# Kernel tuning notes

Hardware: AMD Instinct MI355X
Metric: run time of the kernel (lower is better)

## Reference

```python
import jax, jax.numpy as jnp
import numpy as np


def setup_inputs() -> dict:
    key = jax.random.key(0)
    k1, k2, k3 = jax.random.split(key, 3)
    B, T, F = 16, 2048, 64
    he = jax.random.normal(k1, (B, T, F), dtype=jnp.float32)
    scale = 1.0 / np.sqrt(F).astype(np.float32)
    W1 = jax.random.normal(k2, (F, F), dtype=jnp.float32) * scale
    W2 = jax.random.normal(k3, (F, F), dtype=jnp.float32) * scale
    return {"he": he, "W1": W1, "W2": W2, "attention_len": 48}


def reference(he, W1, W2, attention_len):
    # he: [B, T, F] encoder states. For each output step i the original module:
    #   1) unrolls L_i = min(attention_len, max(i,1)) decoder steps starting
    #      from he[:, i, :]:  H_k = sigmoid(H_{k-1} @ W1), Y_k = sigmoid(H_k @ W2)
    #   2) attends Y_1..Y_{L_i} against the encoder window he[:, i-L_i:i, :]
    #      with per-step dot-product scores, softmax over the window, and a
    #      weighted sum of the encoder window.
    # (i=0 degenerates to a single-element softmax -> context = he[:, 0, :].)
    B, T, F = he.shape
    A = attention_len

    def step(H, _):
        H = jax.nn.sigmoid(H @ W1)          # [B, T, F]
        Y = jax.nn.sigmoid(H @ W2)          # [B, T, F]
        return H, Y

    # Decoder outputs for every start position, all A steps: Ys[b, i, t, f]
    _, Ys = jax.lax.scan(step, he, None, length=A)   # [A, B, T, F]
    Ys = jnp.moveaxis(Ys, 0, 2)                      # [B, T, A, F]

    i = jnp.arange(T)[:, None]                       # [T, 1]
    t = jnp.arange(A)[None, :]                       # [1, A]
    L = jnp.minimum(A, jnp.maximum(i, 1))            # window length per step
    j = jnp.clip(i - L + t, 0, T - 1)                # encoder index per (i, t)
    valid = t < L                                    # [T, A]

    gathered = he[:, j, :]                           # [B, T, A, F] windowed encoder
    scores = jnp.einsum('btaf,btaf->bta', Ys, gathered)
    scores = jnp.where(valid[None, :, :], scores, jnp.float32(-1e9))
    w = jax.nn.softmax(scores, axis=-1)              # [B, T, A]
    ctx = jnp.einsum('bta,btaf->btf', w, gathered)   # [B, T, F]
    return ctx
```

## Files before the change

kernel.cpp:

```cpp
#include <hip/hip_runtime.h>

#define B_   16
#define T_   2048
#define F_   64
#define A_   48
#define TOK  64
#define WSTR 68
#define HWS  72
#define SSTR 49
#define NWIN 111

typedef __attribute__((ext_vector_type(4))) _Float16 half4;
typedef __attribute__((ext_vector_type(2))) _Float16 half2;
typedef __attribute__((ext_vector_type(4))) float    f32x4;

#define LOG2E 1.4426950408889634f

__device__ __forceinline__ float sigp(float c) {
    return __builtin_amdgcn_rcpf(1.0f + __builtin_amdgcn_exp2f(c));
}
__device__ __forceinline__ half2 pk2(float a, float b) {
    return __builtin_bit_cast(half2, __builtin_amdgcn_cvt_pkrtz(a, b));
}
__device__ __forceinline__ half4 sigpack(f32x4 c) {
    half2 lo = pk2(sigp(c[0]), sigp(c[1]));
    half2 hi = pk2(sigp(c[2]), sigp(c[3]));
    half4 h; h[0] = lo[0]; h[1] = lo[1]; h[2] = hi[0]; h[3] = hi[1];
    return h;
}

__device__ __forceinline__ void gemm4(const half4 (&aW)[4][4], const half4 (&hb)[4], f32x4 (&c)[4]) {
#pragma unroll
    for (int mo = 0; mo < 4; ++mo) {
        f32x4 z = {0.f, 0.f, 0.f, 0.f};
#pragma unroll
        for (int kt = 0; kt < 4; ++kt)
            z = __builtin_amdgcn_mfma_f32_16x16x16f16(aW[mo][kt], hb[kt], z, 0, 0, 0);
        c[mo] = z;
    }
}

struct Smem {
    float    sWin[NWIN * WSTR];
    _Float16 sWinH[NWIN * HWS];
    float    sSc[TOK * SSTR];
};

template<bool FIRST>
__device__ __forceinline__ void run_block(Smem& sm, int b, int t0,
                                          const float* __restrict__ he,
                                          const float* __restrict__ W1,
                                          const float* __restrict__ W2,
                                          float* __restrict__ out)
{
    const int tid = threadIdx.x;
    const float* __restrict__ heB = he + (size_t)b * T_ * F_;

    for (int i = tid; i < NWIN * 16; i += 256) {
        int row = i >> 4, c4 = (i & 15) * 4;
        int g = t0 - 48 + row;
        if (!FIRST || g >= 0) {
            float4 v = *(const float4*)(heB + (size_t)g * F_ + c4);
            *(float4*)(&sm.sWin[row * WSTR + c4]) = v;
            half2 lo = pk2(v.x, v.y), hi = pk2(v.z, v.w);
            half4 h; h[0] = lo[0]; h[1] = lo[1]; h[2] = hi[0]; h[3] = hi[1];
            *(half4*)(&sm.sWinH[row * HWS + c4]) = h;
        }
    }

    const int lane = tid & 63;
    const int wv   = tid >> 6;
    const int quad = lane >> 4;
    const int ml   = lane & 15;
    const int tw0  = wv * 16;
    const int tg   = t0 + tw0 + ml;
    const int L    = min(A_, max(tg, 1));

    half4 aW1[4][4], aW2[4][4];
    for (int mo = 0; mo < 4; ++mo)
        for (int kt = 0; kt < 4; ++kt) {
            half4 f1, f2;
#pragma unroll
            for (int j = 0; j < 4; ++j) {
                int k = kt * 16 + quad * 4 + j;
                f1[j] = (_Float16)(-LOG2E * W1[k * F_ + mo * 16 + ml]);
                f2[j] = (_Float16)(-LOG2E * W2[k * F_ + mo * 16 + ml]);
            }
            aW1[mo][kt] = f1; aW2[mo][kt] = f2;
        }

    half4 hb[4];
#pragma unroll
    for (int kt = 0; kt < 4; ++kt) {
        float4 v = *(const float4*)(heB + (size_t)tg * F_ + kt * 16 + quad * 4);
        half4 h;
        h[0] = (_Float16)v.x; h[1] = (_Float16)v.y;
        h[2] = (_Float16)v.z; h[3] = (_Float16)v.w;
        hb[kt] = h;
    }

    f32x4 c1[4];
    gemm4(aW1, hb, c1);

    __syncthreads();

    const bool amDiag = (quad == (ml >> 2));
    const bool s0 = (ml & 3) == 0, s1 = (ml & 3) == 1, s2 = (ml & 3) == 2;
    float* scp = &sm.sSc[(tw0 + ml) * SSTR];

    const _Float16* __restrict__ wbase = &sm.sWinH[(tw0 + ml) * HWS + quad * 4];

    auto wp_for = [&](int a2) -> const _Float16* {
        if (FIRST) {
            int j = tg - L + a2; if (j < 0) j = 0;
            return &sm.sWinH[(j + 48) * HWS + quad * 4];
        }
        return wbase + a2 * HWS;
    };

    half4 g0, g1, g2, g3;
    {
        const _Float16* wp = wp_for(0);
        g0 = *(const half4*)(wp);
        g1 = *(const half4*)(wp + 16);
        g2 = *(const half4*)(wp + 32);
        g3 = *(const half4*)(wp + 48);
    }

#pragma unroll 4
    for (int a = 0; a < A_; ++a) {
#pragma unroll
        for (int mo = 0; mo < 4; ++mo) hb[mo] = sigpack(c1[mo]);

        f32x4 c2[4];
        gemm4(aW2, hb, c2);
        gemm4(aW1, hb, c1);

        half4 n0, n1, n2, n3;
        {
            int an = (a + 1 < A_) ? a + 1 : A_ - 1;
            const _Float16* wp = wp_for(an);
            n0 = *(const half4*)(wp);
            n1 = *(const half4*)(wp + 16);
            n2 = *(const half4*)(wp + 32);
            n3 = *(const half4*)(wp + 48);
        }

        half4 yh[4];
#pragma unroll
        for (int mo = 0; mo < 4; ++mo) yh[mo] = sigpack(c2[mo]);

        f32x4 za = {0.f, 0.f, 0.f, 0.f}, zb = {0.f, 0.f, 0.f, 0.f};
        za = __builtin_amdgcn_mfma_f32_16x16x16f16(yh[0], g0, za, 0, 0, 0);
        zb = __builtin_amdgcn_mfma_f32_16x16x16f16(yh[1], g1, zb, 0, 0, 0);
        za = __builtin_amdgcn_mfma_f32_16x16x16f16(yh[2], g2, za, 0, 0, 0);
        zb = __builtin_amdgcn_mfma_f32_16x16x16f16(yh[3], g3, zb, 0, 0, 0);
        f32x4 zs = za + zb;
        float val = s0 ? zs[0] : (s1 ? zs[1] : (s2 ? zs[2] : zs[3]));
        if (FIRST) val = (a < L) ? val : -1e9f;
        if (amDiag) scp[a] = val;

        g0 = n0; g1 = n1; g2 = n2; g3 = n3;
    }
    __syncthreads();

    {
        int r = tid >> 2, s = tid & 3;
        float sc[12];
#pragma unroll
        for (int i = 0; i < 12; ++i) sc[i] = sm.sSc[r * SSTR + i * 4 + s];
        float m = sc[0];
#pragma unroll
        for (int i = 1; i < 12; ++i) m = fmaxf(m, sc[i]);
        m = fmaxf(m, __shfl_xor(m, 1));
        m = fmaxf(m, __shfl_xor(m, 2));
        float e[12]; float sum = 0.f;
#pragma unroll
        for (int i = 0; i < 12; ++i) { e[i] = __expf(sc[i] - m); sum += e[i]; }
        sum += __shfl_xor(sum, 1);
        sum += __shfl_xor(sum, 2);
        float inv = __builtin_amdgcn_rcpf(sum);
#pragma unroll
        for (int i = 0; i < 12; ++i) sm.sSc[r * SSTR + i * 4 + s] = e[i] * inv;
    }
    __syncthreads();

    {
        int r = tid >> 2, fc = (tid & 3) * 16;
        int tgr = t0 + r;
        int Lr = min(A_, max(tgr, 1));
        float acc[16];
#pragma unroll
        for (int q = 0; q < 16; ++q) acc[q] = 0.f;
        for (int a = 0; a < A_; ++a) {
            float wgt = sm.sSc[r * SSTR + a];
            int j = tgr - Lr + a;
            if (FIRST) { if (j < 0) j = 0; }
            const float* wp = &sm.sWin[(j - t0 + 48) * WSTR + fc];
#pragma unroll
            for (int q = 0; q < 4; ++q) {
                float4 g = *(const float4*)(wp + q * 4);
                acc[q*4+0] += wgt * g.x; acc[q*4+1] += wgt * g.y;
                acc[q*4+2] += wgt * g.z; acc[q*4+3] += wgt * g.w;
            }
        }
        float* op = out + ((size_t)b * T_ + tgr) * F_ + fc;
#pragma unroll
        for (int q = 0; q < 4; ++q)
            *(float4*)(op + q * 4) = make_float4(acc[q*4], acc[q*4+1], acc[q*4+2], acc[q*4+3]);
    }
}

__global__ __launch_bounds__(256)
void ContextBlock_kernel(const float* __restrict__ he, const float* __restrict__ W1,
                         const float* __restrict__ W2, float* __restrict__ out)
{
    __shared__ Smem sm;
    const int blk = blockIdx.x;
    if (blk < B_ * 31) {
        int b  = blk / 31;
        int t0 = ((blk % 31) + 1) * TOK;
        run_block<false>(sm, b, t0, he, W1, W2, out);
    } else {
        int b = blk - B_ * 31;
        run_block<true>(sm, b, 0, he, W1, W2, out);
    }
}

extern "C" void kernel_launch(void* const* d_in, const int* in_sizes, int n_in,
                              void* d_out, int out_size, void* d_ws, size_t ws_size,
                              hipStream_t stream) {
    const float* he = (const float*)d_in[0];
    const float* W1 = (const float*)d_in[1];
    const float* W2 = (const float*)d_in[2];
    float* out = (float*)d_out;
    hipLaunchKernelGGL(ContextBlock_kernel, dim3(512), dim3(256), 0, stream, he, W1, W2, out);
}
```

Measured before the change: 124.9 us.

## Process two token groups per wave to interleave independent MFMA recurrence chains

Each wave now handles 32 tokens as two independent 16-token groups, interleaving their sigmoid/MFMA recurrence chains to hide dependency latency within a wave. The block size is halved to 128 threads, and the window load, softmax and weighted-sum phases are remapped to cover 64 tokens with fewer threads. This trades thread-level parallelism and occupancy for instruction-level parallelism and higher register use per thread.

```diff
diff --git a/kernel.cpp b/kernel.cpp
--- a/kernel.cpp
+++ b/kernel.cpp
@@ -56,7 +56,7 @@
     const int tid = threadIdx.x;
     const float* __restrict__ heB = he + (size_t)b * T_ * F_;
 
-    for (int i = tid; i < NWIN * 16; i += 256) {
+    for (int i = tid; i < NWIN * 16; i += 128) {
         int row = i >> 4, c4 = (i & 15) * 4;
         int g = t0 - 48 + row;
         if (!FIRST || g >= 0) {
@@ -72,9 +72,11 @@
     const int wv   = tid >> 6;
     const int quad = lane >> 4;
     const int ml   = lane & 15;
-    const int tw0  = wv * 16;
-    const int tg   = t0 + tw0 + ml;
-    const int L    = min(A_, max(tg, 1));
+    const int tw0  = wv * 32;
+    const int tgA  = t0 + tw0 + ml;
+    const int tgB  = tgA + 16;
+    const int LA   = min(A_, max(tgA, 1));
+    const int LB   = min(A_, max(tgB, 1));
 
     half4 aW1[4][4], aW2[4][4];
     for (int mo = 0; mo < 4; ++mo)
@@ -89,116 +91,157 @@
             aW1[mo][kt] = f1; aW2[mo][kt] = f2;
         }
 
-    half4 hb[4];
+    half4 hbA[4], hbB[4];
 #pragma unroll
     for (int kt = 0; kt < 4; ++kt) {
-        float4 v = *(const float4*)(heB + (size_t)tg * F_ + kt * 16 + quad * 4);
+        float4 v = *(const float4*)(heB + (size_t)tgA * F_ + kt * 16 + quad * 4);
         half4 h;
         h[0] = (_Float16)v.x; h[1] = (_Float16)v.y;
         h[2] = (_Float16)v.z; h[3] = (_Float16)v.w;
-        hb[kt] = h;
-    }
-
-    f32x4 c1[4];
-    gemm4(aW1, hb, c1);
+        hbA[kt] = h;
+        float4 w = *(const float4*)(heB + (size_t)tgB * F_ + kt * 16 + quad * 4);
+        half4 g;
+        g[0] = (_Float16)w.x; g[1] = (_Float16)w.y;
+        g[2] = (_Float16)w.z; g[3] = (_Float16)w.w;
+        hbB[kt] = g;
+    }
+
+    f32x4 c1A[4], c1B[4];
+    gemm4(aW1, hbA, c1A);
+    gemm4(aW1, hbB, c1B);
 
     __syncthreads();
 
     const bool amDiag = (quad == (ml >> 2));
     const bool s0 = (ml & 3) == 0, s1 = (ml & 3) == 1, s2 = (ml & 3) == 2;
-    float* scp = &sm.sSc[(tw0 + ml) * SSTR];
-
-    const _Float16* __restrict__ wbase = &sm.sWinH[(tw0 + ml) * HWS + quad * 4];
-
-    auto wp_for = [&](int a2) -> const _Float16* {
+    float* scpA = &sm.sSc[(tw0 + ml) * SSTR];
+    float* scpB = &sm.sSc[(tw0 + 16 + ml) * SSTR];
+
+    const _Float16* __restrict__ wbaseA = &sm.sWinH[(tw0 + ml) * HWS + quad * 4];
+    const _Float16* __restrict__ wbaseB = &sm.sWinH[(tw0 + 16 + ml) * HWS + quad * 4];
+
+    auto wpA_for = [&](int a2) -> const _Float16* {
         if (FIRST) {
-            int j = tg - L + a2; if (j < 0) j = 0;
+            int j = tgA - LA + a2; if (j < 0) j = 0;
             return &sm.sWinH[(j + 48) * HWS + quad * 4];
         }
-        return wbase + a2 * HWS;
+        return wbaseA + a2 * HWS;
     };
-
-    half4 g0, g1, g2, g3;
+    auto wpB_for = [&](int a2) -> const _Float16* {
+        if (FIRST) {
+            int j = tgB - LB + a2; if (j < 0) j = 0;
+            return &sm.sWinH[(j + 48) * HWS + quad * 4];
+        }
+        return wbaseB + a2 * HWS;
+    };
+
+    half4 gA0, gA1, gA2, gA3, gB0, gB1, gB2, gB3;
     {
-        const _Float16* wp = wp_for(0);
-        g0 = *(const half4*)(wp);
-        g1 = *(const half4*)(wp + 16);
-        g2 = *(const half4*)(wp + 32);
-        g3 = *(const half4*)(wp + 48);
-    }
-
-#pragma unroll 4
+        const _Float16* wp = wpA_for(0);
+        gA0 = *(const half4*)(wp);
+        gA1 = *(const half4*)(wp + 16);
+        gA2 = *(const half4*)(wp + 32);
+        gA3 = *(const half4*)(wp + 48);
+        wp = wpB_for(0);
+        gB0 = *(const half4*)(wp);
+        gB1 = *(const half4*)(wp + 16);
+        gB2 = *(const half4*)(wp + 32);
+        gB3 = *(const half4*)(wp + 48);
+    }
+
+#pragma unroll 2
     for (int a = 0; a < A_; ++a) {
 #pragma unroll
-        for (int mo = 0; mo < 4; ++mo) hb[mo] = sigpack(c1[mo]);
-
-        f32x4 c2[4];
-        gemm4(aW2, hb, c2);
-        gemm4(aW1, hb, c1);
-
-        half4 n0, n1, n2, n3;
+        for (int mo = 0; mo < 4; ++mo) hbA[mo] = sigpack(c1A[mo]);
+#pragma unroll
+        for (int mo = 0; mo < 4; ++mo) hbB[mo] = sigpack(c1B[mo]);
+
+        f32x4 c2A[4], c2B[4];
+        gemm4(aW2, hbA, c2A);
+        gemm4(aW2, hbB, c2B);
+        gemm4(aW1, hbA, c1A);
+        gemm4(aW1, hbB, c1B);
+
+        int an = (a + 1 < A_) ? a + 1 : A_ - 1;
+        half4 nA0, nA1, nA2, nA3, nB0, nB1, nB2, nB3;
         {
-            int an = (a + 1 < A_) ? a + 1 : A_ - 1;
-            const _Float16* wp = wp_for(an);
-            n0 = *(const half4*)(wp);
-            n1 = *(const half4*)(wp + 16);
-            n2 = *(const half4*)(wp + 32);
-            n3 = *(const half4*)(wp + 48);
-        }
-
-        half4 yh[4];
-#pragma unroll
-        for (int mo = 0; mo < 4; ++mo) yh[mo] = sigpack(c2[mo]);
-
-        f32x4 za = {0.f, 0.f, 0.f, 0.f}, zb = {0.f, 0.f, 0.f, 0.f};
-        za = __builtin_amdgcn_mfma_f32_16x16x16f16(yh[0], g0, za, 0, 0, 0);
-        zb = __builtin_amdgcn_mfma_f32_16x16x16f16(yh[1], g1, zb, 0, 0, 0);
-        za = __builtin_amdgcn_mfma_f32_16x16x16f16(yh[2], g2, za, 0, 0, 0);
-        zb = __builtin_amdgcn_mfma_f32_16x16x16f16(yh[3], g3, zb, 0, 0, 0);
-        f32x4 zs = za + zb;
-        float val = s0 ? zs[0] : (s1 ? zs[1] : (s2 ? zs[2] : zs[3]));
-        if (FIRST) val = (a < L) ? val : -1e9f;
-        if (amDiag) scp[a] = val;
-
-        g0 = n0; g1 = n1; g2 = n2; g3 = n3;
+            const _Float16* wp = wpA_for(an);
+            nA0 = *(const half4*)(wp);
+            nA1 = *(const half4*)(wp + 16);
+            nA2 = *(const half4*)(wp + 32);
+            nA3 = *(const half4*)(wp + 48);
+            wp = wpB_for(an);
+            nB0 = *(const half4*)(wp);
+            nB1 = *(const half4*)(wp + 16);
+            nB2 = *(const half4*)(wp + 32);
+            nB3 = *(const half4*)(wp + 48);
+        }
+
+        half4 yhA[4], yhB[4];
+#pragma unroll
+        for (int mo = 0; mo < 4; ++mo) yhA[mo] = sigpack(c2A[mo]);
+#pragma unroll
+        for (int mo = 0; mo < 4; ++mo) yhB[mo] = sigpack(c2B[mo]);
+
+        f32x4 zaA = {0.f,0.f,0.f,0.f}, zbA = {0.f,0.f,0.f,0.f};
+        zaA = __builtin_amdgcn_mfma_f32_16x16x16f16(yhA[0], gA0, zaA, 0, 0, 0);
+        zbA = __builtin_amdgcn_mfma_f32_16x16x16f16(yhA[1], gA1, zbA, 0, 0, 0);
+        zaA = __builtin_amdgcn_mfma_f32_16x16x16f16(yhA[2], gA2, zaA, 0, 0, 0);
+        zbA = __builtin_amdgcn_mfma_f32_16x16x16f16(yhA[3], gA3, zbA, 0, 0, 0);
+        f32x4 zaB = {0.f,0.f,0.f,0.f}, zbB = {0.f,0.f,0.f,0.f};
+        zaB = __builtin_amdgcn_mfma_f32_16x16x16f16(yhB[0], gB0, zaB, 0, 0, 0);
+        zbB = __builtin_amdgcn_mfma_f32_16x16x16f16(yhB[1], gB1, zbB, 0, 0, 0);
+        zaB = __builtin_amdgcn_mfma_f32_16x16x16f16(yhB[2], gB2, zaB, 0, 0, 0);
+        zbB = __builtin_amdgcn_mfma_f32_16x16x16f16(yhB[3], gB3, zbB, 0, 0, 0);
+
+        f32x4 zsA = zaA + zbA;
+        float valA = s0 ? zsA[0] : (s1 ? zsA[1] : (s2 ? zsA[2] : zsA[3]));
+        if (FIRST) valA = (a < LA) ? valA : -1e9f;
+        if (amDiag) scpA[a] = valA;
+
+        f32x4 zsB = zaB + zbB;
+        float valB = s0 ? zsB[0] : (s1 ? zsB[1] : (s2 ? zsB[2] : zsB[3]));
+        if (FIRST) valB = (a < LB) ? valB : -1e9f;
+        if (amDiag) scpB[a] = valB;
+
+        gA0 = nA0; gA1 = nA1; gA2 = nA2; gA3 = nA3;
+        gB0 = nB0; gB1 = nB1; gB2 = nB2; gB3 = nB3;
     }
     __syncthreads();
 
     {
-        int r = tid >> 2, s = tid & 3;
-        float sc[12];
-#pragma unroll
-        for (int i = 0; i < 12; ++i) sc[i] = sm.sSc[r * SSTR + i * 4 + s];
+        int r = tid >> 1, s = tid & 1;
+        float sc[24];
+#pragma unroll
+        for (int i = 0; i < 24; ++i) sc[i] = sm.sSc[r * SSTR + i * 2 + s];
         float m = sc[0];
 #pragma unroll
-        for (int i = 1; i < 12; ++i) m = fmaxf(m, sc[i]);
+        for (int i = 1; i < 24; ++i) m = fmaxf(m, sc[i]);
         m = fmaxf(m, __shfl_xor(m, 1));
-        m = fmaxf(m, __shfl_xor(m, 2));
-        float e[12]; float sum = 0.f;
-#pragma unroll
-        for (int i = 0; i < 12; ++i) { e[i] = __expf(sc[i] - m); sum += e[i]; }
+        float e[24]; float sum = 0.f;
+#pragma unroll
+        for (int i = 0; i < 24; ++i) { e[i] = __expf(sc[i] - m); sum += e[i]; }
         sum += __shfl_xor(sum, 1);
-        sum += __shfl_xor(sum, 2);
         float inv = __builtin_amdgcn_rcpf(sum);
 #pragma unroll
-        for (int i = 0; i < 12; ++i) sm.sSc[r * SSTR + i * 4 + s] = e[i] * inv;
+        for (int i = 0; i < 24; ++i) sm.sSc[r * SSTR + i * 2 + s] = e[i] * inv;
     }
     __syncthreads();
 
     {
-        int r = tid >> 2, fc = (tid & 3) * 16;
+        int r = tid >> 1, fc = (tid & 1) * 32;
         int tgr = t0 + r;
         int Lr = min(A_, max(tgr, 1));
-        float acc[16];
-#pragma unroll
-        for (int q = 0; q < 16; ++q) acc[q] = 0.f;
+        float acc[32];
+#pragma unroll
+        for (int q = 0; q < 32; ++q) acc[q] = 0.f;
         for (int a = 0; a < A_; ++a) {
             float wgt = sm.sSc[r * SSTR + a];
             int j = tgr - Lr + a;
             if (FIRST) { if (j < 0) j = 0; }
             const float* wp = &sm.sWin[(j - t0 + 48) * WSTR + fc];
 #pragma unroll
-            for (int q = 0; q < 4; ++q) {
+            for (int q = 0; q < 8; ++q) {
                 float4 g = *(const float4*)(wp + q * 4);
                 acc[q*4+0] += wgt * g.x; acc[q*4+1] += wgt * g.y;
                 acc[q*4+2] += wgt * g.z; acc[q*4+3] += wgt * g.w;
@@ -206,12 +249,12 @@
         }
         float* op = out + ((size_t)b * T_ + tgr) * F_ + fc;
 #pragma unroll
-        for (int q = 0; q < 4; ++q)
+        for (int q = 0; q < 8; ++q)
             *(float4*)(op + q * 4) = make_float4(acc[q*4], acc[q*4+1], acc[q*4+2], acc[q*4+3]);
     }
 }
 
-__global__ __launch_bounds__(256)
+__global__ __launch_bounds__(128, 1)
 void ContextBlock_kernel(const float* __restrict__ he, const float* __restrict__ W1,
                          const float* __restrict__ W2, float* __restrict__ out)
 {
@@ -234,5 +277,5 @@
     const float* W1 = (const float*)d_in[1];
     const float* W2 = (const float*)d_in[2];
     float* out = (float*)d_out;
-    hipLaunchKernelGGL(ContextBlock_kernel, dim3(512), dim3(256), 0, stream, he, W1, W2, out);
-}
+    hipLaunchKernelGGL(ContextBlock_kernel, dim3(512), dim3(128), 0, stream, he, W1, W2, out);
+}
```

Result: slower. 128.3 us (+2.7%).

## Switch recurrence to 32x32x8 MFMA with 32 tokens per wave, 128-thread blocks

Applied to the files above, without the earlier changes.

The decoder recurrence and score computation move from 16x16x16 MFMA tiles (16 tokens per wave, 4 waves) to 32x32x8 tiles (32 tokens per wave, 2 waves per 64-token block). The block size drops to 128 threads, and softmax and context accumulation are reorganized to two threads per row. The larger MFMA tile cuts instruction count per FLOP and changes register layout. In exchange it raises register pressure (32 accumulators, 8 window fragments) and halves waves per block, which could reduce latency hiding on the serial sigmoid chain.

```diff
diff --git a/kernel.cpp b/kernel.cpp
--- a/kernel.cpp
+++ b/kernel.cpp
@@ -10,33 +10,36 @@
 #define SSTR 49
 #define NWIN 111
 
-typedef __attribute__((ext_vector_type(4))) _Float16 half4;
-typedef __attribute__((ext_vector_type(2))) _Float16 half2;
-typedef __attribute__((ext_vector_type(4))) float    f32x4;
+typedef __attribute__((ext_vector_type(4)))  _Float16 half4;
+typedef __attribute__((ext_vector_type(2)))  _Float16 h2;
+typedef __attribute__((ext_vector_type(4)))  float    f32x4;
+typedef __attribute__((ext_vector_type(16))) float    f32x16;
 
 #define LOG2E 1.4426950408889634f
 
 __device__ __forceinline__ float sigp(float c) {
     return __builtin_amdgcn_rcpf(1.0f + __builtin_amdgcn_exp2f(c));
 }
-__device__ __forceinline__ half2 pk2(float a, float b) {
-    return __builtin_bit_cast(half2, __builtin_amdgcn_cvt_pkrtz(a, b));
-}
-__device__ __forceinline__ half4 sigpack(f32x4 c) {
-    half2 lo = pk2(sigp(c[0]), sigp(c[1]));
-    half2 hi = pk2(sigp(c[2]), sigp(c[3]));
+__device__ __forceinline__ h2 pk2(float a, float b) {
+    return __builtin_bit_cast(h2, __builtin_amdgcn_cvt_pkrtz(a, b));
+}
+template<int G>
+__device__ __forceinline__ half4 sig4(const f32x16& c) {
+    h2 lo = pk2(sigp(c[4*G+0]), sigp(c[4*G+1]));
+    h2 hi = pk2(sigp(c[4*G+2]), sigp(c[4*G+3]));
     half4 h; h[0] = lo[0]; h[1] = lo[1]; h[2] = hi[0]; h[3] = hi[1];
     return h;
 }
 
-__device__ __forceinline__ void gemm4(const half4 (&aW)[4][4], const half4 (&hb)[4], f32x4 (&c)[4]) {
-#pragma unroll
-    for (int mo = 0; mo < 4; ++mo) {
-        f32x4 z = {0.f, 0.f, 0.f, 0.f};
-#pragma unroll
-        for (int kt = 0; kt < 4; ++kt)
-            z = __builtin_amdgcn_mfma_f32_16x16x16f16(aW[mo][kt], hb[kt], z, 0, 0, 0);
-        c[mo] = z;
+__device__ __forceinline__ void gemm2x8(const half4 (&aW)[2][8], const half4 (&hb)[8],
+                                        f32x16 (&c)[2]) {
+#pragma unroll
+    for (int ct = 0; ct < 2; ++ct) {
+        f32x16 z = 0.f;
+#pragma unroll
+        for (int kt = 0; kt < 8; ++kt)
+            z = __builtin_amdgcn_mfma_f32_32x32x8f16(aW[ct][kt], hb[kt], z, 0, 0, 0);
+        c[ct] = z;
     }
 }
 
@@ -56,13 +59,13 @@
     const int tid = threadIdx.x;
     const float* __restrict__ heB = he + (size_t)b * T_ * F_;
 
-    for (int i = tid; i < NWIN * 16; i += 256) {
+    for (int i = tid; i < NWIN * 16; i += 128) {
         int row = i >> 4, c4 = (i & 15) * 4;
         int g = t0 - 48 + row;
         if (!FIRST || g >= 0) {
             float4 v = *(const float4*)(heB + (size_t)g * F_ + c4);
             *(float4*)(&sm.sWin[row * WSTR + c4]) = v;
-            half2 lo = pk2(v.x, v.y), hi = pk2(v.z, v.w);
+            h2 lo = pk2(v.x, v.y), hi = pk2(v.z, v.w);
             half4 h; h[0] = lo[0]; h[1] = lo[1]; h[2] = hi[0]; h[3] = hi[1];
             *(half4*)(&sm.sWinH[row * HWS + c4]) = h;
         }
@@ -70,148 +73,153 @@
 
     const int lane = tid & 63;
     const int wv   = tid >> 6;
-    const int quad = lane >> 4;
-    const int ml   = lane & 15;
-    const int tw0  = wv * 16;
-    const int tg   = t0 + tw0 + ml;
+    const int hi   = lane >> 5;
+    const int tok  = lane & 31;
+    const int tw0  = wv * 32;
+    const int tg   = t0 + tw0 + tok;
     const int L    = min(A_, max(tg, 1));
 
-    half4 aW1[4][4], aW2[4][4];
-    for (int mo = 0; mo < 4; ++mo)
-        for (int kt = 0; kt < 4; ++kt) {
+    half4 aW1[2][8], aW2[2][8];
+    for (int ct = 0; ct < 2; ++ct)
+        for (int kt = 0; kt < 8; ++kt) {
             half4 f1, f2;
 #pragma unroll
             for (int j = 0; j < 4; ++j) {
-                int k = kt * 16 + quad * 4 + j;
-                f1[j] = (_Float16)(-LOG2E * W1[k * F_ + mo * 16 + ml]);
-                f2[j] = (_Float16)(-LOG2E * W2[k * F_ + mo * 16 + ml]);
+                int k = kt * 8 + hi * 4 + j;
+                f1[j] = (_Float16)(-LOG2E * W1[k * F_ + ct * 32 + tok]);
+                f2[j] = (_Float16)(-LOG2E * W2[k * F_ + ct * 32 + tok]);
             }
-            aW1[mo][kt] = f1; aW2[mo][kt] = f2;
-        }
-
-    half4 hb[4];
-#pragma unroll
-    for (int kt = 0; kt < 4; ++kt) {
-        float4 v = *(const float4*)(heB + (size_t)tg * F_ + kt * 16 + quad * 4);
-        half4 h;
-        h[0] = (_Float16)v.x; h[1] = (_Float16)v.y;
-        h[2] = (_Float16)v.z; h[3] = (_Float16)v.w;
+            aW1[ct][kt] = f1; aW2[ct][kt] = f2;
+        }
+
+    half4 hb[8];
+#pragma unroll
+    for (int kt = 0; kt < 8; ++kt) {
+        float4 v = *(const float4*)(heB + (size_t)tg * F_ + kt * 8 + hi * 4);
+        half4 h; h[0] = (_Float16)v.x; h[1] = (_Float16)v.y;
+                 h[2] = (_Float16)v.z; h[3] = (_Float16)v.w;
         hb[kt] = h;
     }
 
-    f32x4 c1[4];
-    gemm4(aW1, hb, c1);
+    f32x16 c1[2];
+    gemm2x8(aW1, hb, c1);
 
     __syncthreads();
 
-    const bool amDiag = (quad == (ml >> 2));
-    const bool s0 = (ml & 3) == 0, s1 = (ml & 3) == 1, s2 = (ml & 3) == 2;
-    float* scp = &sm.sSc[(tw0 + ml) * SSTR];
-
-    const _Float16* __restrict__ wbase = &sm.sWinH[(tw0 + ml) * HWS + quad * 4];
+    const bool amDiag = (hi == ((tok >> 2) & 1));
+    const bool q0 = (tok & 3) == 0, q1 = (tok & 3) == 1, q2 = (tok & 3) == 2;
+    const bool b3 = ((tok >> 3) & 1) != 0, b4 = ((tok >> 4) & 1) != 0;
+    float* scp = &sm.sSc[(tw0 + tok) * SSTR];
+
+    const _Float16* __restrict__ wrow = &sm.sWinH[(tw0 + tok) * HWS + hi * 4];
 
     auto wp_for = [&](int a2) -> const _Float16* {
         if (FIRST) {
             int j = tg - L + a2; if (j < 0) j = 0;
-            return &sm.sWinH[(j + 48) * HWS + quad * 4];
-        }
-        return wbase + a2 * HWS;
+            return &sm.sWinH[(j + 48) * HWS + hi * 4];
+        }
+        return wrow + a2 * HWS;
     };
 
-    half4 g0, g1, g2, g3;
+    half4 g[8];
     {
         const _Float16* wp = wp_for(0);
-        g0 = *(const half4*)(wp);
-        g1 = *(const half4*)(wp + 16);
-        g2 = *(const half4*)(wp + 32);
-        g3 = *(const half4*)(wp + 48);
-    }
-
-#pragma unroll 4
+#pragma unroll
+        for (int kt = 0; kt < 8; ++kt) g[kt] = *(const half4*)(wp + kt * 8);
+    }
+
+#pragma unroll 2
     for (int a = 0; a < A_; ++a) {
-#pragma unroll
-        for (int mo = 0; mo < 4; ++mo) hb[mo] = sigpack(c1[mo]);
-
-        f32x4 c2[4];
-        gemm4(aW2, hb, c2);
-        gemm4(aW1, hb, c1);
-
-        half4 n0, n1, n2, n3;
+        hb[0] = sig4<0>(c1[0]); hb[1] = sig4<1>(c1[0]);
+        hb[2] = sig4<2>(c1[0]); hb[3] = sig4<3>(c1[0]);
+        hb[4] = sig4<0>(c1[1]); hb[5] = sig4<1>(c1[1]);
+        hb[6] = sig4<2>(c1[1]); hb[7] = sig4<3>(c1[1]);
+
+        f32x16 c2[2];
+        gemm2x8(aW2, hb, c2);
+        gemm2x8(aW1, hb, c1);
+
+        half4 gn[8];
         {
             int an = (a + 1 < A_) ? a + 1 : A_ - 1;
             const _Float16* wp = wp_for(an);
-            n0 = *(const half4*)(wp);
-            n1 = *(const half4*)(wp + 16);
-            n2 = *(const half4*)(wp + 32);
-            n3 = *(const half4*)(wp + 48);
-        }
-
-        half4 yh[4];
-#pragma unroll
-        for (int mo = 0; mo < 4; ++mo) yh[mo] = sigpack(c2[mo]);
-
-        f32x4 za = {0.f, 0.f, 0.f, 0.f}, zb = {0.f, 0.f, 0.f, 0.f};
-        za = __builtin_amdgcn_mfma_f32_16x16x16f16(yh[0], g0, za, 0, 0, 0);
-        zb = __builtin_amdgcn_mfma_f32_16x16x16f16(yh[1], g1, zb, 0, 0, 0);
-        za = __builtin_amdgcn_mfma_f32_16x16x16f16(yh[2], g2, za, 0, 0, 0);
-        zb = __builtin_amdgcn_mfma_f32_16x16x16f16(yh[3], g3, zb, 0, 0, 0);
-        f32x4 zs = za + zb;
-        float val = s0 ? zs[0] : (s1 ? zs[1] : (s2 ? zs[2] : zs[3]));
+#pragma unroll
+            for (int kt = 0; kt < 8; ++kt) gn[kt] = *(const half4*)(wp + kt * 8);
+        }
+
+        half4 yh[8];
+        yh[0] = sig4<0>(c2[0]); yh[1] = sig4<1>(c2[0]);
+        yh[2] = sig4<2>(c2[0]); yh[3] = sig4<3>(c2[0]);
+        yh[4] = sig4<0>(c2[1]); yh[5] = sig4<1>(c2[1]);
+        yh[6] = sig4<2>(c2[1]); yh[7] = sig4<3>(c2[1]);
+
+        f32x16 zs = 0.f;
+#pragma unroll
+        for (int kt = 0; kt < 8; ++kt)
+            zs = __builtin_amdgcn_mfma_f32_32x32x8f16(yh[kt], g[kt], zs, 0, 0, 0);
+
+        f32x4 h0 = {zs[0],  zs[1],  zs[2],  zs[3]};
+        f32x4 h1 = {zs[4],  zs[5],  zs[6],  zs[7]};
+        f32x4 h2v = {zs[8],  zs[9],  zs[10], zs[11]};
+        f32x4 h3 = {zs[12], zs[13], zs[14], zs[15]};
+        f32x4 sA = b3 ? h1 : h0;
+        f32x4 sB = b3 ? h3 : h2v;
+        f32x4 sC = b4 ? sB : sA;
+        float val = q0 ? sC[0] : (q1 ? sC[1] : (q2 ? sC[2] : sC[3]));
         if (FIRST) val = (a < L) ? val : -1e9f;
         if (amDiag) scp[a] = val;
 
-        g0 = n0; g1 = n1; g2 = n2; g3 = n3;
+#pragma unroll
+        for (int kt = 0; kt < 8; ++kt) g[kt] = gn[kt];
     }
     __syncthreads();
 
     {
-        int r = tid >> 2, s = tid & 3;
-        float sc[12];
-#pragma unroll
-        for (int i = 0; i < 12; ++i) sc[i] = sm.sSc[r * SSTR + i * 4 + s];
+        int r = tid >> 1, s = tid & 1;
+        float sc[24];
+#pragma unroll
+        for (int i = 0; i < 24; ++i) sc[i] = sm.sSc[r * SSTR + i * 2 + s];
         float m = sc[0];
 #pragma unroll
-        for (int i = 1; i < 12; ++i) m = fmaxf(m, sc[i]);
+        for (int i = 1; i < 24; ++i) m = fmaxf(m, sc[i]);
         m = fmaxf(m, __shfl_xor(m, 1));
-        m = fmaxf(m, __shfl_xor(m, 2));
-        float e[12]; float sum = 0.f;
-#pragma unroll
-        for (int i = 0; i < 12; ++i) { e[i] = __expf(sc[i] - m); sum += e[i]; }
+        float e[24]; float sum = 0.f;
+#pragma unroll
+        for (int i = 0; i < 24; ++i) { e[i] = __expf(sc[i] - m); sum += e[i]; }
         sum += __shfl_xor(sum, 1);
-        sum += __shfl_xor(sum, 2);
         float inv = __builtin_amdgcn_rcpf(sum);
 #pragma unroll
-        for (int i = 0; i < 12; ++i) sm.sSc[r * SSTR + i * 4 + s] = e[i] * inv;
+        for (int i = 0; i < 24; ++i) sm.sSc[r * SSTR + i * 2 + s] = e[i] * inv;
     }
     __syncthreads();
 
     {
-        int r = tid >> 2, fc = (tid & 3) * 16;
+        int r = tid >> 1, fc = (tid & 1) * 32;
         int tgr = t0 + r;
         int Lr = min(A_, max(tgr, 1));
-        float acc[16];
-#pragma unroll
-        for (int q = 0; q < 16; ++q) acc[q] = 0.f;
+        float acc[32];
+#pragma unroll
+        for (int q = 0; q < 32; ++q) acc[q] = 0.f;
         for (int a = 0; a < A_; ++a) {
             float wgt = sm.sSc[r * SSTR + a];
             int j = tgr - Lr + a;
             if (FIRST) { if (j < 0) j = 0; }
             const float* wp = &sm.sWin[(j - t0 + 48) * WSTR + fc];
 #pragma unroll
-            for (int q = 0; q < 4; ++q) {
-                float4 g = *(const float4*)(wp + q * 4);
-                acc[q*4+0] += wgt * g.x; acc[q*4+1] += wgt * g.y;
-                acc[q*4+2] += wgt * g.z; acc[q*4+3] += wgt * g.w;
+            for (int q = 0; q < 8; ++q) {
+                float4 gv = *(const float4*)(wp + q * 4);
+                acc[q*4+0] += wgt * gv.x; acc[q*4+1] += wgt * gv.y;
+                acc[q*4+2] += wgt * gv.z; acc[q*4+3] += wgt * gv.w;
             }
         }
         float* op = out + ((size_t)b * T_ + tgr) * F_ + fc;
 #pragma unroll
-        for (int q = 0; q < 4; ++q)
+        for (int q = 0; q < 8; ++q)
             *(float4*)(op + q * 4) = make_float4(acc[q*4], acc[q*4+1], acc[q*4+2], acc[q*4+3]);
     }
 }
 
-__global__ __launch_bounds__(256)
+__global__ __launch_bounds__(128, 1)
 void ContextBlock_kernel(const float* __restrict__ he, const float* __restrict__ W1,
                          const float* __restrict__ W2, float* __restrict__ out)
 {
@@ -234,5 +242,5 @@
     const float* W1 = (const float*)d_in[1];
     const float* W2 = (const float*)d_in[2];
     float* out = (float*)d_out;
-    hipLaunchKernelGGL(ContextBlock_kernel, dim3(512), dim3(256), 0, stream, he, W1, W2, out);
-}
+    hipLaunchKernelGGL(ContextBlock_kernel, dim3(512), dim3(128), 0, stream, he, W1, W2, out);
+}
```

Result: slower. 130.7 us (+4.6%).
